# Kernel optimization log

Hardware: AMD Instinct MI355X
Metric: run time of the kernel (lower is better)

## Reference

```python
import jax, jax.numpy as jnp
import numpy as np

T, B, V, D, H, C = 2048, 32, 50257, 512, 768, 10


def setup_inputs() -> dict:
    key = jax.random.key(0)
    ks = jax.random.split(key, 11)
    s = 0.02
    return {
        "x": jax.random.randint(ks[0], (T, B), 0, V),
        "embed_table": jax.random.normal(ks[1], (V, D), jnp.float32) * s,
        "W_x": jax.random.normal(ks[2], (H, D), jnp.float32) * s,
        "W_f": jax.random.normal(ks[3], (H, D), jnp.float32) * s,
        "b_f": jax.random.normal(ks[4], (H,), jnp.float32) * s,
        "W_r": jax.random.normal(ks[5], (H, D), jnp.float32) * s,
        "b_r": jax.random.normal(ks[6], (H,), jnp.float32) * s,
        "W_cx": jax.random.normal(ks[7], (H, D), jnp.float32) * s,
        "b_cx": jax.random.normal(ks[8], (H,), jnp.float32) * s,
        "W_out": jax.random.normal(ks[9], (C, H), jnp.float32) * s,
        "b_out": jax.random.normal(ks[10], (C,), jnp.float32) * s,
    }


def reference(x, embed_table, W_x, W_f, b_f, W_r, b_r, W_cx, b_cx, W_out, b_out):
    # Embedding lookup: [T, B, D]
    e = embed_table[x]
    # Precompute all gate projections for every timestep (batched GEMMs).
    xp = jnp.einsum("tbd,hd->tbh", e, W_x)                 # x_t projection
    f = jax.nn.sigmoid(jnp.einsum("tbd,hd->tbh", e, W_f) + b_f)   # forget gate
    r = jax.nn.sigmoid(jnp.einsum("tbd,hd->tbh", e, W_r) + b_r)   # reset gate
    cx = jnp.einsum("tbd,hd->tbh", e, W_cx) + b_cx                # highway path

    c0 = jnp.zeros((B, H), e.dtype)  # init_hidden: zeros

    def step(c, inp):
        f_t, xp_t, r_t, cx_t = inp
        c = f_t * c + (1.0 - f_t) * xp_t
        h = r_t * jnp.tanh(c) + (1.0 - r_t) * cx_t
        return c, h

    _, ht = jax.lax.scan(step, c0, (f, xp, r, cx))  # ht: [T, B, H]

    # tanh -> max-pool over time -> tanh -> classifier
    pooled = jnp.max(jnp.tanh(ht), axis=0)          # [B, H]
    pooled = jnp.tanh(pooled)
    logit = pooled @ W_out.T + b_out                # [B, C]
    return logit
```

## Files before the change

### kernel.cpp

```cpp
#include <hip/hip_runtime.h>
#include <hip/hip_bf16.h>
#include <cstdint>
#include <cstddef>

#define T_DIM 2048
#define B_DIM 32
#define D_DIM 512
#define H_DIM 768
#define C_DIM 10
#define K_DIM D_DIM
#define N_DIM (4 * H_DIM)

#define TC 1024
#define NCHUNK (T_DIM / TC)
#define MC (TC * B_DIM)

#define L_SEG 64
#define S_SEG (TC / L_SEG)
#define BH (B_DIM * H_DIM)

typedef __attribute__((ext_vector_type(8))) short short8;
typedef __attribute__((ext_vector_type(4))) float float4v;

__device__ inline unsigned short f2bf(float f) {
  unsigned int u = __builtin_bit_cast(unsigned int, f);
  unsigned int r = (u + 0x7FFFu + ((u >> 16) & 1u)) >> 16;
  return (unsigned short)r;
}
__device__ inline float bf2f(unsigned short s) {
  unsigned int u = ((unsigned int)s) << 16;
  return __builtin_bit_cast(float, u);
}
__device__ inline float fast_rcp(float x) { return __builtin_amdgcn_rcpf(x); }
__device__ inline float fast_exp2(float x) { return __builtin_amdgcn_exp2f(x); }
__device__ inline float sigmoid_f(float x) {
  float e = fast_exp2(-1.4426950408889634f * x);
  return fast_rcp(1.0f + e);
}
__device__ inline float tanh_f(float x) {
  float e = fast_exp2(2.885390081777927f * x);
  return 1.0f - 2.0f * fast_rcp(e + 1.0f);
}
__device__ inline void gld16(const unsigned short* g, unsigned short* l) {
  __builtin_amdgcn_global_load_lds(
      (const __attribute__((address_space(1))) void*)g,
      (__attribute__((address_space(3))) void*)l, 16, 0, 0);
}
__device__ inline unsigned int pack_bf16x2(float lo, float hi) {
  return ((unsigned int)f2bf(hi) << 16) | (unsigned int)f2bf(lo);
}

__global__ __launch_bounds__(256) void gather_embed_kernel(
    const int* __restrict__ x_c, const float* __restrict__ table,
    unsigned short* __restrict__ ebfc) {
  int idx = blockIdx.x * 256 + threadIdx.x;
  int m = idx >> 7;
  int k4 = (idx & 127) << 2;
  int row = x_c[m];
  float4 v = *(const float4*)(table + (size_t)row * D_DIM + k4);
  ushort4 o;
  o.x = f2bf(v.x); o.y = f2bf(v.y); o.z = f2bf(v.z); o.w = f2bf(v.w);
  *(ushort4*)(ebfc + (size_t)m * D_DIM + k4) = o;
}

__global__ __launch_bounds__(256) void convert_w_kernel(
    const float* __restrict__ Wx, const float* __restrict__ Wf,
    const float* __restrict__ Wr, const float* __restrict__ Wcx,
    unsigned short* __restrict__ wcat) {
  int idx = blockIdx.x * 256 + threadIdx.x;
  int n = idx >> 7;
  int k4 = (idx & 127) << 2;
  int mat = n / H_DIM;
  int h = n - mat * H_DIM;
  const float* src = (mat == 0) ? Wx : (mat == 1) ? Wf : (mat == 2) ? Wr : Wcx;
  float4 v = *(const float4*)(src + (size_t)h * D_DIM + k4);
  ushort4 o;
  o.x = f2bf(v.x); o.y = f2bf(v.y); o.z = f2bf(v.z); o.w = f2bf(v.w);
  *(ushort4*)(wcat + (size_t)n * D_DIM + k4) = o;
}

#define BM 128
#define BN 128
#define BK 32

__global__ __launch_bounds__(256, 4) void gemm_kernel(
    const unsigned short* __restrict__ ebfc,
    const unsigned short* __restrict__ wcat,
    const float* __restrict__ b_f, const float* __restrict__ b_r,
    const float* __restrict__ b_cx,
    unsigned short* __restrict__ projc) {
  __shared__ __align__(16) unsigned short smem[16384];
  unsigned short* As0 = smem;
  unsigned short* As1 = smem + 4096;
  unsigned short* Bs0 = smem + 8192;
  unsigned short* Bs1 = smem + 12288;

  int tid  = threadIdx.x;
  int wave = tid >> 6;
  int lane = tid & 63;
  int quad = lane >> 4;
  int l16  = lane & 15;
  int m0 = blockIdx.y * BM;
  int n0 = blockIdx.x * BN;
  int wn = (wave & 1) * 64;
  int wm = (wave >> 1) * 64;

  int row0 = tid >> 2;
  int cl0  = (tid & 3) ^ ((row0 >> 1) & 3);

  const unsigned short* gA0 = ebfc + (size_t)(m0 + row0) * K_DIM + cl0 * 8;
  const unsigned short* gB0 = wcat + (size_t)(n0 + row0) * K_DIM + cl0 * 8;
  const unsigned short* gA1 = gA0 + (size_t)64 * K_DIM;
  const unsigned short* gB1 = gB0 + (size_t)64 * K_DIM;

  float4v acc[4][4] = {};

#define STAGE(Adst, Bdst, kt) do { \
    gld16(gA0 + (kt), (Adst) + tid * 8); \
    gld16(gB0 + (kt), (Bdst) + tid * 8); \
    gld16(gA1 + (kt), (Adst) + 2048 + tid * 8); \
    gld16(gB1 + (kt), (Bdst) + 2048 + tid * 8); } while (0)

  STAGE(As0, Bs0, 0);
  __syncthreads();

#pragma unroll
  for (int ki = 0; ki < K_DIM / BK; ki++) {
    unsigned short* Ac = (ki & 1) ? As1 : As0;
    unsigned short* Bc = (ki & 1) ? Bs1 : Bs0;
    if (ki + 1 < K_DIM / BK) {
      unsigned short* An = (ki & 1) ? As0 : As1;
      unsigned short* Bn = (ki & 1) ? Bs0 : Bs1;
      STAGE(An, Bn, (ki + 1) * BK);
    }
    short8 wf[4], ef[4];
#pragma unroll
    for (int i = 0; i < 4; i++) {
      int r = wn + i * 16 + l16;
      int p = quad ^ ((r >> 1) & 3);
      wf[i] = *(const short8*)(Bc + r * BK + p * 8);
    }
#pragma unroll
    for (int j = 0; j < 4; j++) {
      int r = wm + j * 16 + l16;
      int p = quad ^ ((r >> 1) & 3);
      ef[j] = *(const short8*)(Ac + r * BK + p * 8);
    }
#pragma unroll
    for (int i = 0; i < 4; i++)
#pragma unroll
      for (int j = 0; j < 4; j++)
        acc[i][j] = __builtin_amdgcn_mfma_f32_16x16x32_bf16(wf[i], ef[j], acc[i][j], 0, 0, 0);
    __syncthreads();
  }

  int mat = n0 / H_DIM;
  int hb = n0 - mat * H_DIM;
  size_t matBase = (size_t)mat * MC * H_DIM;
  const float* bias = (mat == 1) ? b_f : (mat == 2) ? b_r : b_cx;
#pragma unroll
  for (int i = 0; i < 4; i++) {
    int hl = wn + i * 16 + quad * 4;
    float4 bv;
    if (mat == 0) { bv.x = bv.y = bv.z = bv.w = 0.0f; }
    else          { bv = *(const float4*)(bias + hb + hl); }
#pragma unroll
    for (int j = 0; j < 4; j++) {
      int row = wm + j * 16 + l16;
      float v0 = acc[i][j][0] + bv.x;
      float v1 = acc[i][j][1] + bv.y;
      float v2 = acc[i][j][2] + bv.z;
      float v3 = acc[i][j][3] + bv.w;
      if (mat == 1 || mat == 2) {
        v0 = sigmoid_f(v0); v1 = sigmoid_f(v1);
        v2 = sigmoid_f(v2); v3 = sigmoid_f(v3);
      }
      uint2 pk;
      pk.x = pack_bf16x2(v0, v1);
      pk.y = pack_bf16x2(v2, v3);
      int chunk = (hl >> 3) ^ (row & 7);
      *(uint2*)(smem + row * 128 + chunk * 8 + (hl & 7)) = pk;
    }
  }
  __syncthreads();
#pragma unroll
  for (int s = 0; s < 8; s++) {
    int idx = s * 256 + tid;
    int row = idx >> 4;
    int ck  = idx & 15;
    int phys = ck ^ (row & 7);
    short8 v = *(const short8*)(smem + row * 128 + phys * 8);
    *(short8*)(projc + matBase + (size_t)(m0 + row) * H_DIM + hb + ck * 8) = v;
  }
}

__global__ __launch_bounds__(128) void scan1_kernel(
    const unsigned short* __restrict__ projc,
    float* __restrict__ Pw, float* __restrict__ Qw) {
  int blk = blockIdx.x;
  int seg = blk / (BH / 512);
  int q   = blk % (BH / 512);
  int e4  = (q * 128 + threadIdx.x) * 4;
  const size_t mstr = (size_t)MC * H_DIM;
  size_t idx0 = (size_t)(seg * L_SEG) * BH + e4;
  float p0 = 1.f, p1 = 1.f, p2 = 1.f, p3 = 1.f;
  float c0 = 0.f, c1 = 0.f, c2 = 0.f, c3 = 0.f;
#pragma unroll 4
  for (int t = 0; t < L_SEG; t++) {
    size_t id = idx0 + (size_t)t * BH;
    ushort4 xp = *(const ushort4*)(projc + id);
    ushort4 ff = *(const ushort4*)(projc + mstr + id);
    float f0 = bf2f(ff.x), f1 = bf2f(ff.y), f2 = bf2f(ff.z), f3 = bf2f(ff.w);
    c0 = fmaf(f0, c0 - bf2f(xp.x), bf2f(xp.x));
    c1 = fmaf(f1, c1 - bf2f(xp.y), bf2f(xp.y));
    c2 = fmaf(f2, c2 - bf2f(xp.z), bf2f(xp.z));
    c3 = fmaf(f3, c3 - bf2f(xp.w), bf2f(xp.w));
    p0 *= f0; p1 *= f1; p2 *= f2; p3 *= f3;
  }
  int o = seg * BH + e4;
  *(float4*)(Pw + o) = make_float4(p0, p1, p2, p3);
  *(float4*)(Qw + o) = make_float4(c0, c1, c2, c3);
}

__global__ __launch_bounds__(256) void prefix_kernel(
    const float* __restrict__ Pw, const float* __restrict__ Qw,
    float* __restrict__ cin, float* __restrict__ c_state,
    const float* __restrict__ segmax, float* __restrict__ hm_state,
    int first, int hm_init) {
  int gid = blockIdx.x * 256 + threadIdx.x;
  float c = first ? 0.f : c_state[gid];
#pragma unroll
  for (int s = 0; s < S_SEG; s++) {
    cin[s * BH + gid] = c;
    c = fmaf(Pw[s * BH + gid], c, Qw[s * BH + gid]);
  }
  c_state[gid] = c;
  if (!first) {
    float m = segmax[gid];
#pragma unroll
    for (int s = 1; s < S_SEG; s++) m = fmaxf(m, segmax[s * BH + gid]);
    hm_state[gid] = hm_init ? m : fmaxf(hm_state[gid], m);
  }
}

__global__ __launch_bounds__(128) void scan2_kernel(
    const unsigned short* __restrict__ projc,
    const float* __restrict__ cin, float* __restrict__ segmax) {
  int blk = blockIdx.x;
  int seg = blk / (BH / 512);
  int q   = blk % (BH / 512);
  int e4  = (q * 128 + threadIdx.x) * 4;
  const size_t mstr = (size_t)MC * H_DIM;
  size_t idx0 = (size_t)(seg * L_SEG) * BH + e4;
  int o = seg * BH + e4;
  float4 cv = *(const float4*)(cin + o);
  float c0 = cv.x, c1 = cv.y, c2 = cv.z, c3 = cv.w;
  float m0 = -1e30f, m1 = -1e30f, m2 = -1e30f, m3 = -1e30f;
#pragma unroll 2
  for (int t = 0; t < L_SEG; t++) {
    size_t id = idx0 + (size_t)t * BH;
    ushort4 xp = *(const ushort4*)(projc + id);
    ushort4 ff = *(const ushort4*)(projc + mstr + id);
    ushort4 rr = *(const ushort4*)(projc + 2 * mstr + id);
    ushort4 cx = *(const ushort4*)(projc + 3 * mstr + id);
    c0 = fmaf(bf2f(ff.x), c0 - bf2f(xp.x), bf2f(xp.x));
    c1 = fmaf(bf2f(ff.y), c1 - bf2f(xp.y), bf2f(xp.y));
    c2 = fmaf(bf2f(ff.z), c2 - bf2f(xp.z), bf2f(xp.z));
    c3 = fmaf(bf2f(ff.w), c3 - bf2f(xp.w), bf2f(xp.w));
    float h0 = fmaf(bf2f(rr.x), tanh_f(c0) - bf2f(cx.x), bf2f(cx.x));
    float h1 = fmaf(bf2f(rr.y), tanh_f(c1) - bf2f(cx.y), bf2f(cx.y));
    float h2 = fmaf(bf2f(rr.z), tanh_f(c2) - bf2f(cx.z), bf2f(cx.z));
    float h3 = fmaf(bf2f(rr.w), tanh_f(c3) - bf2f(cx.w), bf2f(cx.w));
    m0 = fmaxf(m0, h0); m1 = fmaxf(m1, h1);
    m2 = fmaxf(m2, h2); m3 = fmaxf(m3, h3);
  }
  *(float4*)(segmax + o) = make_float4(m0, m1, m2, m3);
}

__global__ __launch_bounds__(256) void pool_final_kernel(
    const float* __restrict__ segmax, const float* __restrict__ hm_state,
    float* __restrict__ pooled) {
  int gid = blockIdx.x * 256 + threadIdx.x;
  float m = hm_state[gid];
#pragma unroll
  for (int s = 0; s < S_SEG; s++) m = fmaxf(m, segmax[s * BH + gid]);
  pooled[gid] = tanh_f(tanh_f(m));
}

__global__ __launch_bounds__(64) void classifier_kernel(
    const float* __restrict__ pooled, const float* __restrict__ W_out,
    const float* __restrict__ b_out, float* __restrict__ out) {
  int b = blockIdx.x / C_DIM;
  int c = blockIdx.x % C_DIM;
  int lane = threadIdx.x;
  float s = 0.0f;
#pragma unroll
  for (int i = 0; i < H_DIM / 64; i++) {
    int h = i * 64 + lane;
    s += pooled[(size_t)b * H_DIM + h] * W_out[(size_t)c * H_DIM + h];
  }
#pragma unroll
  for (int off = 32; off; off >>= 1) s += __shfl_down(s, off, 64);
  if (lane == 0) out[b * C_DIM + c] = s + b_out[c];
}

extern "C" void kernel_launch(void* const* d_in, const int* in_sizes, int n_in,
                              void* d_out, int out_size, void* d_ws, size_t ws_size,
                              hipStream_t stream) {
  const int*   x     = (const int*)d_in[0];
  const float* table = (const float*)d_in[1];
  const float* W_x   = (const float*)d_in[2];
  const float* W_f   = (const float*)d_in[3];
  const float* b_f   = (const float*)d_in[4];
  const float* W_r   = (const float*)d_in[5];
  const float* b_r   = (const float*)d_in[6];
  const float* W_cx  = (const float*)d_in[7];
  const float* b_cx  = (const float*)d_in[8];
  const float* W_out = (const float*)d_in[9];
  const float* b_out = (const float*)d_in[10];

  char* ws = (char*)d_ws;
  size_t off = 0;
  unsigned short* wcat  = (unsigned short*)(ws + off); off += (size_t)N_DIM * K_DIM * 2;
  unsigned short* ebfc  = (unsigned short*)(ws + off); off += (size_t)MC * K_DIM * 2;
  unsigned short* projc = (unsigned short*)(ws + off); off += (size_t)4 * MC * H_DIM * 2;
  float* Pw     = (float*)(ws + off); off += (size_t)S_SEG * BH * 4;
  float* Qw     = (float*)(ws + off); off += (size_t)S_SEG * BH * 4;
  float* cin    = (float*)(ws + off); off += (size_t)S_SEG * BH * 4;
  float* segmax = (float*)(ws + off); off += (size_t)S_SEG * BH * 4;
  float* c_st   = (float*)(ws + off); off += (size_t)BH * 4;
  float* hm_st  = (float*)(ws + off); off += (size_t)BH * 4;
  float* pooled = (float*)(ws + off); off += (size_t)BH * 4;

  convert_w_kernel<<<(N_DIM * K_DIM / 4) / 256, 256, 0, stream>>>(W_x, W_f, W_r, W_cx, wcat);

  dim3 g(N_DIM / BN, MC / BM);
  for (int ch = 0; ch < NCHUNK; ch++) {
    gather_embed_kernel<<<(MC * K_DIM / 4) / 256, 256, 0, stream>>>(x + (size_t)ch * MC, table, ebfc);
    gemm_kernel<<<g, 256, 0, stream>>>(ebfc, wcat, b_f, b_r, b_cx, projc);
    scan1_kernel<<<S_SEG * (BH / 512), 128, 0, stream>>>(projc, Pw, Qw);
    prefix_kernel<<<BH / 256, 256, 0, stream>>>(Pw, Qw, cin, c_st, segmax, hm_st,
                                                ch == 0, ch == 1);
    scan2_kernel<<<S_SEG * (BH / 512), 128, 0, stream>>>(projc, cin, segmax);
  }
  pool_final_kernel<<<BH / 256, 256, 0, stream>>>(segmax, hm_st, pooled);
  classifier_kernel<<<B_DIM * C_DIM, 64, 0, stream>>>(pooled, W_out, b_out, (float*)d_out);
}
```

Baseline: 549.1 us.

## Rewrite projection GEMM with 256x256 tiles, 8 waves and interleaved staged pipeline

Replaces the 128x128x32 double-buffered GEMM with a 256x256x64 tile kernel using 512 threads (8 waves), each wave computing a 128x64 subtile. Global-to-LDS loads are split into quarter stages interleaved between MFMA clusters, with explicit barriers, sched_barrier, setprio and vmcnt waits to overlap loads with compute. The larger tile raises arithmetic intensity and cuts redundant global reads. The cost is 128KB of LDS, a heavier register load, and fewer blocks in flight.

```diff
diff --git a/kernel.cpp b/kernel.cpp
--- a/kernel.cpp
+++ b/kernel.cpp
@@ -79,98 +79,181 @@
   *(ushort4*)(wcat + (size_t)n * D_DIM + k4) = o;
 }
 
-#define BM 128
-#define BN 128
-#define BK 32
-
-__global__ __launch_bounds__(256, 4) void gemm_kernel(
+#define BMT 256
+#define BNT 256
+#define BKT 64
+#define NTILES (K_DIM / BKT)
+
+__device__ __forceinline__ float4v mfma16(short8 a, short8 b, float4v c) {
+  return __builtin_amdgcn_mfma_f32_16x16x32_bf16(a, b, c, 0, 0, 0);
+}
+
+__device__ __forceinline__ void stg(const unsigned short* src, unsigned short* sm,
+                                    int pb, int isB, int h, int kt, int tid) {
+  const unsigned short* s = src + (size_t)(h * 128) * K_DIM + kt * BKT;
+  unsigned short* d = sm + pb * 32768 + isB * 16384 + h * 8192 + tid * 8;
+  gld16(s, d);
+  gld16(s + (size_t)64 * K_DIM, d + 4096);
+}
+
+template <int S1, int S2, int S3, int S4, int VMN>
+__device__ __forceinline__ void tile_step(
+    int u, unsigned short* sm, const unsigned short* srcA,
+    const unsigned short* srcB, int tid, int aO, int bO, int c0, int c1,
+    float4v (&acc)[8][4]) {
+  const int pb = u & 1, pn = pb ^ 1;
+  const int ab = pb * 32768 + aO;
+  const int bb = pb * 32768 + bO;
+  short8 a[4][2], b0[2][2], b1[2][2];
+
+#pragma unroll
+  for (int f = 0; f < 4; f++) {
+    a[f][0] = *(const short8*)(sm + ab + f * 1024 + c0);
+    a[f][1] = *(const short8*)(sm + ab + f * 1024 + c1);
+  }
+#pragma unroll
+  for (int g = 0; g < 2; g++) {
+    b0[g][0] = *(const short8*)(sm + bb + g * 1024 + c0);
+    b0[g][1] = *(const short8*)(sm + bb + g * 1024 + c1);
+  }
+  if constexpr (S1) stg(srcA, sm, pn, 0, 0, u + 1, tid);
+  __builtin_amdgcn_sched_barrier(0);
+  __builtin_amdgcn_s_barrier();
+  __builtin_amdgcn_s_setprio(1);
+#pragma unroll
+  for (int f = 0; f < 4; f++)
+#pragma unroll
+    for (int g = 0; g < 2; g++) {
+      acc[f][g] = mfma16(a[f][0], b0[g][0], acc[f][g]);
+      acc[f][g] = mfma16(a[f][1], b0[g][1], acc[f][g]);
+    }
+  __builtin_amdgcn_s_setprio(0);
+  __builtin_amdgcn_sched_barrier(0);
+  __builtin_amdgcn_s_barrier();
+
+#pragma unroll
+  for (int g = 0; g < 2; g++) {
+    b1[g][0] = *(const short8*)(sm + bb + 2048 + g * 1024 + c0);
+    b1[g][1] = *(const short8*)(sm + bb + 2048 + g * 1024 + c1);
+  }
+  if constexpr (S2) stg(srcA, sm, pn, 0, 1, u + 1, tid);
+  __builtin_amdgcn_sched_barrier(0);
+  __builtin_amdgcn_s_barrier();
+  __builtin_amdgcn_s_setprio(1);
+#pragma unroll
+  for (int f = 0; f < 4; f++)
+#pragma unroll
+    for (int g = 0; g < 2; g++) {
+      acc[f][2 + g] = mfma16(a[f][0], b1[g][0], acc[f][2 + g]);
+      acc[f][2 + g] = mfma16(a[f][1], b1[g][1], acc[f][2 + g]);
+    }
+  __builtin_amdgcn_s_setprio(0);
+  __builtin_amdgcn_sched_barrier(0);
+  __builtin_amdgcn_s_barrier();
+
+#pragma unroll
+  for (int f = 0; f < 4; f++) {
+    a[f][0] = *(const short8*)(sm + ab + 4096 + f * 1024 + c0);
+    a[f][1] = *(const short8*)(sm + ab + 4096 + f * 1024 + c1);
+  }
+  if constexpr (S3) stg(srcB, sm, pb, 1, 0, u + 2, tid);
+  __builtin_amdgcn_sched_barrier(0);
+  __builtin_amdgcn_s_barrier();
+  __builtin_amdgcn_s_setprio(1);
+#pragma unroll
+  for (int f = 0; f < 4; f++)
+#pragma unroll
+    for (int g = 0; g < 2; g++) {
+      acc[4 + f][2 + g] = mfma16(a[f][0], b1[g][0], acc[4 + f][2 + g]);
+      acc[4 + f][2 + g] = mfma16(a[f][1], b1[g][1], acc[4 + f][2 + g]);
+    }
+  __builtin_amdgcn_s_setprio(0);
+  __builtin_amdgcn_sched_barrier(0);
+  __builtin_amdgcn_s_barrier();
+
+  if constexpr (S4) stg(srcB, sm, pb, 1, 1, u + 2, tid);
+  __builtin_amdgcn_sched_barrier(0);
+  __builtin_amdgcn_s_barrier();
+  __builtin_amdgcn_s_setprio(1);
+#pragma unroll
+  for (int f = 0; f < 4; f++)
+#pragma unroll
+    for (int g = 0; g < 2; g++) {
+      acc[4 + f][g] = mfma16(a[f][0], b0[g][0], acc[4 + f][g]);
+      acc[4 + f][g] = mfma16(a[f][1], b0[g][1], acc[4 + f][g]);
+    }
+  __builtin_amdgcn_s_setprio(0);
+  __builtin_amdgcn_sched_barrier(0);
+  if constexpr (VMN == 4)
+    asm volatile("s_waitcnt vmcnt(4)" ::: "memory");
+  else if constexpr (VMN == 0)
+    asm volatile("s_waitcnt vmcnt(0)" ::: "memory");
+  __builtin_amdgcn_s_barrier();
+}
+
+__global__ __launch_bounds__(512, 2) void gemm_kernel(
     const unsigned short* __restrict__ ebfc,
     const unsigned short* __restrict__ wcat,
     const float* __restrict__ b_f, const float* __restrict__ b_r,
     const float* __restrict__ b_cx,
     unsigned short* __restrict__ projc) {
-  __shared__ __align__(16) unsigned short smem[16384];
-  unsigned short* As0 = smem;
-  unsigned short* As1 = smem + 4096;
-  unsigned short* Bs0 = smem + 8192;
-  unsigned short* Bs1 = smem + 12288;
-
-  int tid  = threadIdx.x;
-  int wave = tid >> 6;
-  int lane = tid & 63;
-  int quad = lane >> 4;
-  int l16  = lane & 15;
-  int m0 = blockIdx.y * BM;
-  int n0 = blockIdx.x * BN;
-  int wn = (wave & 1) * 64;
-  int wm = (wave >> 1) * 64;
-
-  int row0 = tid >> 2;
-  int cl0  = (tid & 3) ^ ((row0 >> 1) & 3);
-
-  const unsigned short* gA0 = ebfc + (size_t)(m0 + row0) * K_DIM + cl0 * 8;
-  const unsigned short* gB0 = wcat + (size_t)(n0 + row0) * K_DIM + cl0 * 8;
-  const unsigned short* gA1 = gA0 + (size_t)64 * K_DIM;
-  const unsigned short* gB1 = gB0 + (size_t)64 * K_DIM;
-
-  float4v acc[4][4] = {};
-
-#define STAGE(Adst, Bdst, kt) do { \
-    gld16(gA0 + (kt), (Adst) + tid * 8); \
-    gld16(gB0 + (kt), (Bdst) + tid * 8); \
-    gld16(gA1 + (kt), (Adst) + 2048 + tid * 8); \
-    gld16(gB1 + (kt), (Bdst) + 2048 + tid * 8); } while (0)
-
-  STAGE(As0, Bs0, 0);
-  __syncthreads();
-
-#pragma unroll
-  for (int ki = 0; ki < K_DIM / BK; ki++) {
-    unsigned short* Ac = (ki & 1) ? As1 : As0;
-    unsigned short* Bc = (ki & 1) ? Bs1 : Bs0;
-    if (ki + 1 < K_DIM / BK) {
-      unsigned short* An = (ki & 1) ? As0 : As1;
-      unsigned short* Bn = (ki & 1) ? Bs0 : Bs1;
-      STAGE(An, Bn, (ki + 1) * BK);
-    }
-    short8 wf[4], ef[4];
-#pragma unroll
-    for (int i = 0; i < 4; i++) {
-      int r = wn + i * 16 + l16;
-      int p = quad ^ ((r >> 1) & 3);
-      wf[i] = *(const short8*)(Bc + r * BK + p * 8);
-    }
-#pragma unroll
-    for (int j = 0; j < 4; j++) {
-      int r = wm + j * 16 + l16;
-      int p = quad ^ ((r >> 1) & 3);
-      ef[j] = *(const short8*)(Ac + r * BK + p * 8);
-    }
-#pragma unroll
-    for (int i = 0; i < 4; i++)
-#pragma unroll
-      for (int j = 0; j < 4; j++)
-        acc[i][j] = __builtin_amdgcn_mfma_f32_16x16x32_bf16(wf[i], ef[j], acc[i][j], 0, 0, 0);
-    __syncthreads();
-  }
+  __shared__ __align__(16) unsigned short smem[65536];
+
+  const int tid = threadIdx.x;
+  const int wave = tid >> 6;
+  const int lane = tid & 63;
+  const int quad = lane >> 4;
+  const int l16 = lane & 15;
+  const int wn = wave >> 2;
+  const int wm = wave & 3;
+
+  const int n0 = blockIdx.x * BNT;
+  const int m0 = blockIdx.y * BMT;
+
+  const int srow = tid >> 3;
+  const int kch = (tid & 7) ^ (srow & 7);
+  const unsigned short* srcA = wcat + (size_t)(n0 + srow) * K_DIM + kch * 8;
+  const unsigned short* srcB = ebfc + (size_t)(m0 + srow) * K_DIM + kch * 8;
+
+  const int aO = wn * 8192 + l16 * 64;
+  const int bO = 16384 + (wm >> 1) * 8192 + (wm & 1) * 4096 + l16 * 64;
+  const int c0 = (quad ^ (lane & 7)) * 8;
+  const int c1 = ((quad ^ (lane & 7)) ^ 4) * 8;
+
+  float4v acc[8][4] = {};
+
+  stg(srcB, smem, 0, 1, 0, 0, tid);
+  stg(srcB, smem, 0, 1, 1, 0, tid);
+  stg(srcA, smem, 0, 0, 0, 0, tid);
+  stg(srcA, smem, 0, 0, 1, 0, tid);
+  stg(srcB, smem, 1, 1, 0, 1, tid);
+  stg(srcB, smem, 1, 1, 1, 1, tid);
+  asm volatile("s_waitcnt vmcnt(4)" ::: "memory");
+  __builtin_amdgcn_s_barrier();
+
+#pragma unroll 2
+  for (int u = 0; u < NTILES - 2; u++)
+    tile_step<1, 1, 1, 1, 4>(u, smem, srcA, srcB, tid, aO, bO, c0, c1, acc);
+  tile_step<1, 1, 0, 0, 0>(NTILES - 2, smem, srcA, srcB, tid, aO, bO, c0, c1, acc);
+  tile_step<0, 0, 0, 0, -1>(NTILES - 1, smem, srcA, srcB, tid, aO, bO, c0, c1, acc);
 
   int mat = n0 / H_DIM;
   int hb = n0 - mat * H_DIM;
   size_t matBase = (size_t)mat * MC * H_DIM;
   const float* bias = (mat == 1) ? b_f : (mat == 2) ? b_r : b_cx;
 #pragma unroll
-  for (int i = 0; i < 4; i++) {
-    int hl = wn + i * 16 + quad * 4;
+  for (int f = 0; f < 8; f++) {
+    int hl = wn * 128 + f * 16 + quad * 4;
     float4 bv;
     if (mat == 0) { bv.x = bv.y = bv.z = bv.w = 0.0f; }
     else          { bv = *(const float4*)(bias + hb + hl); }
 #pragma unroll
-    for (int j = 0; j < 4; j++) {
-      int row = wm + j * 16 + l16;
-      float v0 = acc[i][j][0] + bv.x;
-      float v1 = acc[i][j][1] + bv.y;
-      float v2 = acc[i][j][2] + bv.z;
-      float v3 = acc[i][j][3] + bv.w;
+    for (int g = 0; g < 4; g++) {
+      int ml = wm * 64 + g * 16 + l16;
+      float v0 = acc[f][g][0] + bv.x;
+      float v1 = acc[f][g][1] + bv.y;
+      float v2 = acc[f][g][2] + bv.z;
+      float v3 = acc[f][g][3] + bv.w;
       if (mat == 1 || mat == 2) {
         v0 = sigmoid_f(v0); v1 = sigmoid_f(v1);
         v2 = sigmoid_f(v2); v3 = sigmoid_f(v3);
@@ -178,19 +261,20 @@
       uint2 pk;
       pk.x = pack_bf16x2(v0, v1);
       pk.y = pack_bf16x2(v2, v3);
-      int chunk = (hl >> 3) ^ (row & 7);
-      *(uint2*)(smem + row * 128 + chunk * 8 + (hl & 7)) = pk;
+      int log8 = hl >> 2;
+      int phys8 = log8 ^ ((ml & 7) << 1);
+      *(uint2*)(smem + ml * 256 + phys8 * 4) = pk;
     }
   }
   __syncthreads();
 #pragma unroll
-  for (int s = 0; s < 8; s++) {
-    int idx = s * 256 + tid;
-    int row = idx >> 4;
-    int ck  = idx & 15;
-    int phys = ck ^ (row & 7);
-    short8 v = *(const short8*)(smem + row * 128 + phys * 8);
-    *(short8*)(projc + matBase + (size_t)(m0 + row) * H_DIM + hb + ck * 8) = v;
+  for (int it = 0; it < 16; it++) {
+    int idx = it * 512 + tid;
+    int ml = idx >> 5;
+    int c16 = idx & 31;
+    int phys16 = c16 ^ (ml & 7);
+    short8 v = *(const short8*)(smem + ml * 256 + phys16 * 8);
+    *(short8*)(projc + matBase + (size_t)(m0 + ml) * H_DIM + hb + c16 * 8) = v;
   }
 }
 
@@ -334,10 +418,10 @@
 
   convert_w_kernel<<<(N_DIM * K_DIM / 4) / 256, 256, 0, stream>>>(W_x, W_f, W_r, W_cx, wcat);
 
-  dim3 g(N_DIM / BN, MC / BM);
+  dim3 g(N_DIM / BNT, MC / BMT);
   for (int ch = 0; ch < NCHUNK; ch++) {
     gather_embed_kernel<<<(MC * K_DIM / 4) / 256, 256, 0, stream>>>(x + (size_t)ch * MC, table, ebfc);
-    gemm_kernel<<<g, 256, 0, stream>>>(ebfc, wcat, b_f, b_r, b_cx, projc);
+    gemm_kernel<<<g, 512, 0, stream>>>(ebfc, wcat, b_f, b_r, b_cx, projc);
     scan1_kernel<<<S_SEG * (BH / 512), 128, 0, stream>>>(projc, Pw, Qw);
     prefix_kernel<<<BH / 256, 256, 0, stream>>>(Pw, Qw, cin, c_st, segmax, hm_st,
                                                 ch == 0, ch == 1);
```

New measurement: 553.8 us. Within noise of the previous version (+0.9%).
